# Performance work log

Hardware: AMD Instinct MI355X
Metric: run time of the kernel (lower is better)

The kernel has to match this reference:

```python
import jax, jax.numpy as jnp
import numpy as np

N_NODES = 50000
N_EDGES = 600000
HEADS = 4
DH = 64
NUM_GRAPHS = 8
NEG_SLOPE = 0.2


def setup_inputs() -> dict:
    key = jax.random.key(0)
    ks = jax.random.split(key, 10)
    feat = jax.random.normal(ks[0], (N_NODES, 128), jnp.float32)
    W0 = jax.random.normal(ks[1], (128, HEADS * DH), jnp.float32) * 0.05
    W1 = jax.random.normal(ks[2], (HEADS * DH, HEADS * DH), jnp.float32) * 0.05
    W2 = jax.random.normal(ks[3], (HEADS * DH, HEADS * DH), jnp.float32) * 0.05
    a0 = jax.random.normal(ks[4], (HEADS, DH), jnp.float32) * 0.05
    a1 = jax.random.normal(ks[5], (HEADS, DH), jnp.float32) * 0.05
    a2 = jax.random.normal(ks[6], (HEADS, DH), jnp.float32) * 0.05
    src = jax.random.randint(ks[7], (N_EDGES,), 0, N_NODES, jnp.int32)
    dst = jax.random.randint(ks[8], (N_EDGES,), 0, N_NODES, jnp.int32)
    graph_ids = jnp.sort(jax.random.randint(ks[9], (N_NODES,), 0, NUM_GRAPHS, jnp.int32))
    return {"feat": feat, "W0": W0, "W1": W1, "W2": W2,
            "a0": a0, "a1": a1, "a2": a2,
            "src": src, "dst": dst, "graph_ids": graph_ids}


def _gatv2_layer(h, W, a, src, dst, residual):
    # DGL GATv2Conv with share_weights=True, bias=False, activation=elu.
    n = h.shape[0]
    feat = (h @ W).reshape(n, HEADS, DH)               # (N,H,D)
    # GATv2 attention: score_ij = a . leaky_relu(W h_i + W h_j)
    e = jax.nn.leaky_relu(feat[src] + feat[dst], NEG_SLOPE)  # (E,H,D)
    scores = jnp.einsum('ehd,hd->eh', e, a)            # (E,H)
    # edge softmax over incoming edges of each dst node
    m = jnp.full((n, HEADS), -jnp.inf, scores.dtype).at[dst].max(scores)
    ex = jnp.exp(scores - m[dst])
    denom = jnp.zeros((n, HEADS), scores.dtype).at[dst].add(ex)
    alpha = ex / denom[dst]                            # (E,H)
    out = jnp.zeros((n, HEADS, DH), h.dtype).at[dst].add(alpha[..., None] * feat[src])
    if residual:
        out = out + h.reshape(n, HEADS, DH)            # identity residual (in == H*D)
    return jax.nn.elu(out).reshape(n, HEADS * DH)      # flatten(1)


def reference(feat, W0, W1, W2, a0, a1, a2, src, dst, graph_ids):
    h = _gatv2_layer(feat, W0, a0, src, dst, residual=False)
    h = _gatv2_layer(h, W1, a1, src, dst, residual=True)
    h = _gatv2_layer(h, W2, a2, src, dst, residual=True)
    # dgl.mean_nodes: per-graph mean over nodes
    sums = jax.ops.segment_sum(h, graph_ids, num_segments=NUM_GRAPHS)
    counts = jax.ops.segment_sum(jnp.ones((h.shape[0],), h.dtype), graph_ids,
                                 num_segments=NUM_GRAPHS)
    return sums / jnp.maximum(counts, 1.0)[:, None]    # (NUM_GRAPHS, H*D)
```

## Files before the change

### kernel.cpp

```cpp
#include <hip/hip_runtime.h>
#include <math.h>

#define N_NODES 50000
#define N_EDGES 600000
#define HD 256
#define NUM_GRAPHS 8
#define POOL_CHUNK 128
#define L2E 1.4426950408889634f

static inline size_t align256(size_t x) { return (x + 255) & ~(size_t)255; }

typedef __attribute__((ext_vector_type(8))) short short8;
typedef __attribute__((ext_vector_type(8))) unsigned short u16x8;
typedef __attribute__((ext_vector_type(4))) float f32x4;

__device__ inline float b2f(unsigned short u) {
    union { unsigned int i; float f; } v; v.i = ((unsigned)u) << 16; return v.f;
}
__device__ inline unsigned short f2b(float f) {
    unsigned int u = __float_as_uint(f);
    unsigned int r = (u + 0x7fff + ((u >> 16) & 1)) >> 16;
    return (unsigned short)r;
}

#define CNT_BLOCKS ((N_EDGES + 255) / 256)
__global__ void prep_kernel(const int* __restrict__ dst, int* __restrict__ cnt,
                            const float* __restrict__ W0, const float* __restrict__ W1,
                            const float* __restrict__ W2,
                            unsigned short* __restrict__ Wt0, unsigned short* __restrict__ Wt1,
                            unsigned short* __restrict__ Wt2) {
    __shared__ float t[16][17];
    int b = blockIdx.x;
    if (b < CNT_BLOCKS) {
        int e = b * 256 + threadIdx.x;
        if (e < N_EDGES) atomicAdd(&cnt[dst[e]], 1);
        return;
    }
    b -= CNT_BLOCKS;
    const float* W;
    unsigned short* Wt;
    int K;
    if (b < 128) { W = W0; Wt = Wt0; K = 128; }
    else if (b < 128 + 256) { b -= 128; W = W1; Wt = Wt1; K = 256; }
    else { b -= 384; W = W2; Wt = Wt2; K = 256; }
    const int ktiles = K >> 4;
    const int kt = (b % ktiles) * 16;
    const int nt = (b / ktiles) * 16;
    const int tx = threadIdx.x & 15;
    const int ty = threadIdx.x >> 4;
    t[ty][tx] = W[(size_t)(kt + ty) * HD + nt + tx];
    __syncthreads();
    Wt[(size_t)(nt + ty) * K + kt + tx] = f2b(t[tx][ty]);
}

#define SCAN_BLOCKS ((N_NODES + 256) / 256)
__global__ __launch_bounds__(256) void partial_kernel(const int* __restrict__ cnt,
                                                      int* __restrict__ bsum) {
    __shared__ int ws[4];
    const int lane = threadIdx.x & 63;
    const int wid = threadIdx.x >> 6;
    int i = blockIdx.x * 256 + threadIdx.x;
    int v = (i < N_NODES) ? cnt[i] : 0;
#pragma unroll
    for (int ofs = 32; ofs >= 1; ofs >>= 1) v += __shfl_xor(v, ofs);
    if (lane == 0) ws[wid] = v;
    __syncthreads();
    if (threadIdx.x == 0) bsum[blockIdx.x] = ws[0] + ws[1] + ws[2] + ws[3];
}

__global__ __launch_bounds__(256) void scan2_kernel(const int* __restrict__ cnt,
                                                    const int* __restrict__ bsum,
                                                    int* __restrict__ row_ptr,
                                                    int* __restrict__ cursor) {
    __shared__ int wsum[4];
    __shared__ int s_off;
    const int t = threadIdx.x;
    const int lane = t & 63;
    const int wid = t >> 6;
    const int b = blockIdx.x;
    if (wid == 0) {
        int acc = 0;
        for (int j = lane; j < b; j += 64) acc += bsum[j];
#pragma unroll
        for (int ofs = 32; ofs >= 1; ofs >>= 1) acc += __shfl_xor(acc, ofs);
        if (lane == 0) s_off = acc;
    }
    int i = b * 256 + t;
    int v = (i < N_NODES) ? cnt[i] : 0;
    int x = v;
#pragma unroll
    for (int ofs = 1; ofs < 64; ofs <<= 1) {
        int u = __shfl_up(x, ofs);
        if (lane >= ofs) x += u;
    }
    if (lane == 63) wsum[wid] = x;
    __syncthreads();
    int woff = 0;
#pragma unroll
    for (int j = 0; j < 4; ++j) if (j < wid) woff += wsum[j];
    int excl = s_off + woff + x - v;
    if (i <= N_NODES) { row_ptr[i] = excl; cursor[i] = excl; }
}

__global__ void fill_kernel(const int* __restrict__ src, const int* __restrict__ dst,
                            int* __restrict__ cursor, int* __restrict__ col_src) {
    int e = blockIdx.x * blockDim.x + threadIdx.x;
    if (e < N_EDGES) {
        int d = dst[e];
        int slot = atomicAdd(&cursor[d], 1);
        col_src[slot] = src[e];
    }
}

template<int K, bool AF32>
__global__ __launch_bounds__(256) void mfma_gemm(const void* __restrict__ Ap,
                                                 const unsigned short* __restrict__ Wt,
                                                 unsigned short* __restrict__ C) {
    const int tid = threadIdx.x;
    const int lane = tid & 63;
    const int wave = tid >> 6;
    const int lm = lane & 15;
    const int lk = lane >> 4;
    const int row0 = blockIdx.x * 64;
    const int col0 = wave * 64;

    f32x4 acc[4][4];
#pragma unroll
    for (int rt = 0; rt < 4; ++rt)
#pragma unroll
        for (int ct = 0; ct < 4; ++ct) acc[rt][ct] = (f32x4)(0.f);

    int arow[4];
#pragma unroll
    for (int rt = 0; rt < 4; ++rt) {
        int r = row0 + rt * 16 + lm;
        arow[rt] = r < N_NODES ? r : N_NODES - 1;
    }

    const unsigned short* Ab = (const unsigned short*)Ap;
    const float* Af = (const float*)Ap;

#pragma unroll 2
    for (int k0 = 0; k0 < K; k0 += 32) {
        short8 af[4], bfr[4];
#pragma unroll
        for (int rt = 0; rt < 4; ++rt) {
            if constexpr (AF32) {
                const float* p = &Af[(size_t)arow[rt] * K + k0 + lk * 8];
                float4 v0 = *reinterpret_cast<const float4*>(p);
                float4 v1 = *reinterpret_cast<const float4*>(p + 4);
                short8 a;
                a[0] = (short)f2b(v0.x); a[1] = (short)f2b(v0.y);
                a[2] = (short)f2b(v0.z); a[3] = (short)f2b(v0.w);
                a[4] = (short)f2b(v1.x); a[5] = (short)f2b(v1.y);
                a[6] = (short)f2b(v1.z); a[7] = (short)f2b(v1.w);
                af[rt] = a;
            } else {
                af[rt] = *reinterpret_cast<const short8*>(&Ab[(size_t)arow[rt] * K + k0 + lk * 8]);
            }
        }
#pragma unroll
        for (int ct = 0; ct < 4; ++ct)
            bfr[ct] = *reinterpret_cast<const short8*>(
                &Wt[(size_t)(col0 + ct * 16 + lm) * K + k0 + lk * 8]);
#pragma unroll
        for (int ct = 0; ct < 4; ++ct)
#pragma unroll
            for (int rt = 0; rt < 4; ++rt)
                acc[rt][ct] = __builtin_amdgcn_mfma_f32_16x16x32_bf16(af[rt], bfr[ct], acc[rt][ct], 0, 0, 0);
    }

#pragma unroll
    for (int rt = 0; rt < 4; ++rt)
#pragma unroll
        for (int i = 0; i < 4; ++i) {
            int row = row0 + rt * 16 + lk * 4 + i;
            if (row < N_NODES) {
#pragma unroll
                for (int ct = 0; ct < 4; ++ct)
                    C[(size_t)row * HD + col0 + ct * 16 + lm] = f2b(acc[rt][ct][i]);
            }
        }
}

__global__ __launch_bounds__(256) void aggregate_kernel(
        const unsigned short* __restrict__ feat,
        const float* __restrict__ avec,
        const int* __restrict__ row_ptr,
        const int* __restrict__ col_src,
        unsigned short* __restrict__ hb,
        int residual) {
    const int lane = threadIdx.x & 63;
    const int wave = threadIdx.x >> 6;
    const int half = lane >> 5;
    const int sl = lane & 31;
    const int c0 = sl * 8;
    int n0 = blockIdx.x * 4 + wave;
    if (n0 >= N_NODES) return;
    const int n = __builtin_amdgcn_readfirstlane(n0);

    float av6[8], av4[8];
    {
        float4 v0 = *reinterpret_cast<const float4*>(&avec[c0]);
        float4 v1 = *reinterpret_cast<const float4*>(&avec[c0 + 4]);
        float a[8] = {v0.x, v0.y, v0.z, v0.w, v1.x, v1.y, v1.z, v1.w};
#pragma unroll
        for (int k = 0; k < 8; ++k) {
            av6[k] = a[k] * (0.6f * L2E);
            av4[k] = a[k] * (0.4f * L2E);
        }
    }

    float fd[8];
    {
        u16x8 g = *reinterpret_cast<const u16x8*>(&feat[(size_t)n * HD + c0]);
#pragma unroll
        for (int k = 0; k < 8; ++k) fd[k] = b2f(g[k]);
    }

    const int beg = row_ptr[n];
    const int end = row_ptr[n + 1];

    float denom = 0.f;
    float acc[8];
#pragma unroll
    for (int k = 0; k < 8; ++k) acc[k] = 0.f;

    for (int s = beg; s < end; s += 4) {
        int e0 = col_src[s];
        int e1 = col_src[s + 1];
        int e2 = col_src[s + 2];
        int e3 = col_src[s + 3];
        int eP = half ? e1 : e0;
        int eQ = half ? e3 : e2;
        u16x8 g0 = *reinterpret_cast<const u16x8*>(&feat[(size_t)eP * HD + c0]);
        u16x8 g1 = *reinterpret_cast<const u16x8*>(&feat[(size_t)eQ * HD + c0]);

        float sv0[8], sv1[8];
        float pp0 = 0.f, pp1 = 0.f;
#pragma unroll
        for (int k = 0; k < 8; ++k) {
            sv0[k] = b2f(g0[k]);
            float t = sv0[k] + fd[k];
            pp0 = fmaf(av6[k], t, fmaf(av4[k], fabsf(t), pp0));
        }
#pragma unroll
        for (int k = 0; k < 8; ++k) {
            sv1[k] = b2f(g1[k]);
            float t = sv1[k] + fd[k];
            pp1 = fmaf(av6[k], t, fmaf(av4[k], fabsf(t), pp1));
        }
        pp0 += __shfl_xor(pp0, 1); pp1 += __shfl_xor(pp1, 1);
        pp0 += __shfl_xor(pp0, 2); pp1 += __shfl_xor(pp1, 2);
        pp0 += __shfl_xor(pp0, 4); pp1 += __shfl_xor(pp1, 4);

        float w0 = (s + half < end) ? exp2f(pp0) : 0.f;
        float w1 = (s + 2 + half < end) ? exp2f(pp1) : 0.f;
        denom += w0 + w1;
#pragma unroll
        for (int k = 0; k < 8; ++k)
            acc[k] = fmaf(w0, sv0[k], fmaf(w1, sv1[k], acc[k]));
    }

    denom += __shfl_xor(denom, 32);
#pragma unroll
    for (int k = 0; k < 8; ++k) acc[k] += __shfl_xor(acc[k], 32);

    if (half == 0) {
        const float inv = denom > 0.f ? 1.f / denom : 0.f;
        float o[8];
#pragma unroll
        for (int k = 0; k < 8; ++k) o[k] = acc[k] * inv;
        if (residual) {
            u16x8 hr = *reinterpret_cast<const u16x8*>(&hb[(size_t)n * HD + c0]);
#pragma unroll
            for (int k = 0; k < 8; ++k) o[k] += b2f(hr[k]);
        }
        u16x8 ob;
#pragma unroll
        for (int k = 0; k < 8; ++k) {
            float e = o[k] > 0.f ? o[k] : exp2f(o[k] * L2E) - 1.f;
            ob[k] = f2b(e);
        }
        *reinterpret_cast<u16x8*>(&hb[(size_t)n * HD + c0]) = ob;
    }
}

__global__ __launch_bounds__(256) void pool_kernel(const unsigned short* __restrict__ h,
                                                   const int* __restrict__ gid,
                                                   float* __restrict__ gsums,
                                                   int* __restrict__ gcnt) {
    const int t = threadIdx.x;
    int n0 = blockIdx.x * POOL_CHUNK;
    if (n0 >= N_NODES) return;
    int n1 = n0 + POOL_CHUNK; if (n1 > N_NODES) n1 = N_NODES;
    int curg = gid[n0];
    float sum = 0.f;
    int cnt = 0;
    for (int n = n0; n < n1; ++n) {
        int g = gid[n];
        if (g != curg) {
            atomicAdd(&gsums[(size_t)curg * HD + t], sum);
            if (t == 0) atomicAdd(&gcnt[curg], cnt);
            sum = 0.f; cnt = 0; curg = g;
        }
        sum += b2f(h[(size_t)n * HD + t]);
        ++cnt;
    }
    atomicAdd(&gsums[(size_t)curg * HD + t], sum);
    if (t == 0) atomicAdd(&gcnt[curg], cnt);
}

__global__ void finalize_kernel(const float* __restrict__ gsums,
                                const int* __restrict__ gcnt,
                                float* __restrict__ out) {
    int i = blockIdx.x * blockDim.x + threadIdx.x;
    if (i < NUM_GRAPHS * HD) {
        float c = (float)gcnt[i / HD];
        out[i] = gsums[i] / fmaxf(c, 1.f);
    }
}

extern "C" void kernel_launch(void* const* d_in, const int* in_sizes, int n_in,
                              void* d_out, int out_size, void* d_ws, size_t ws_size,
                              hipStream_t stream) {
    (void)in_sizes; (void)n_in;
    const float* feat = (const float*)d_in[0];
    const float* W0 = (const float*)d_in[1];
    const float* W1 = (const float*)d_in[2];
    const float* W2 = (const float*)d_in[3];
    const float* a0 = (const float*)d_in[4];
    const float* a1 = (const float*)d_in[5];
    const float* a2 = (const float*)d_in[6];
    const int* src = (const int*)d_in[7];
    const int* dst = (const int*)d_in[8];
    const int* gid = (const int*)d_in[9];
    float* out = (float*)d_out;

    char* ws = (char*)d_ws;
    size_t off = 0;
    unsigned short* hb = (unsigned short*)(ws + off);  off = align256(off + (size_t)N_NODES * HD * 2);
    unsigned short* Bh = (unsigned short*)(ws + off);  off = align256(off + (size_t)N_NODES * HD * 2);
    unsigned short* Wt0 = (unsigned short*)(ws + off); off = align256(off + (size_t)HD * 128 * 2);
    unsigned short* Wt1 = (unsigned short*)(ws + off); off = align256(off + (size_t)HD * HD * 2);
    unsigned short* Wt2 = (unsigned short*)(ws + off); off = align256(off + (size_t)HD * HD * 2);
    int* row_ptr = (int*)(ws + off);                   off = align256(off + (size_t)(N_NODES + 1) * 4);
    int* cursor = (int*)(ws + off);                    off = align256(off + (size_t)(N_NODES + 1) * 4);
    int* bsum = (int*)(ws + off);                      off = align256(off + (size_t)SCAN_BLOCKS * 4);
    int* col_src = (int*)(ws + off);                   off = off + (size_t)N_EDGES * 4;
    size_t zstart = off;
    off = align256(off + 16 * 4);
    int* cnt = (int*)(ws + off);                       off = align256(off + (size_t)(N_NODES + 1) * 4);
    float* gsums = (float*)(ws + off);                 off = align256(off + (size_t)NUM_GRAPHS * HD * 4);
    int* gcnt = (int*)(ws + off);                      off = align256(off + (size_t)NUM_GRAPHS * 4);
    size_t zend = off;

    if (ws_size < off) {
        hipMemsetAsync(d_out, 0, (size_t)out_size * 4, stream);
        return;
    }

    hipMemsetAsync(ws + zstart, 0, zend - zstart, stream);

    prep_kernel<<<CNT_BLOCKS + 128 + 256 + 256, 256, 0, stream>>>(
        dst, cnt, W0, W1, W2, Wt0, Wt1, Wt2);
    partial_kernel<<<SCAN_BLOCKS, 256, 0, stream>>>(cnt, bsum);
    scan2_kernel<<<SCAN_BLOCKS, 256, 0, stream>>>(cnt, bsum, row_ptr, cursor);
    fill_kernel<<<(N_EDGES + 255) / 256, 256, 0, stream>>>(src, dst, cursor, col_src);

    const int gemm_blocks = (N_NODES + 63) / 64;
    const int agg_blocks = (N_NODES + 3) / 4;

    mfma_gemm<128, true><<<gemm_blocks, 256, 0, stream>>>(feat, Wt0, Bh);
    aggregate_kernel<<<agg_blocks, 256, 0, stream>>>(Bh, a0, row_ptr, col_src, hb, 0);
    mfma_gemm<256, false><<<gemm_blocks, 256, 0, stream>>>(hb, Wt1, Bh);
    aggregate_kernel<<<agg_blocks, 256, 0, stream>>>(Bh, a1, row_ptr, col_src, hb, 1);
    mfma_gemm<256, false><<<gemm_blocks, 256, 0, stream>>>(hb, Wt2, Bh);
    aggregate_kernel<<<agg_blocks, 256, 0, stream>>>(Bh, a2, row_ptr, col_src, hb, 1);

    pool_kernel<<<(N_NODES + POOL_CHUNK - 1) / POOL_CHUNK, 256, 0, stream>>>(hb, gid, gsums, gcnt);
    finalize_kernel<<<(NUM_GRAPHS * HD + 255) / 256, 256, 0, stream>>>(gsums, gcnt, out);
}
```

Before: 365.0 us.

## Split aggregation into three node-range launches, shrink pool chunk, split score FMAs

Each aggregation layer now runs as three launches over node ranges (0..T1, T1..T2, T2..N) instead of one. The likely aim is to keep each launch's destination working set and row pointer accesses more cache-local. The gathered source features stay random, so the benefit is uncertain, and the split adds launch overhead and a tail at the end of each launch. The score dot product now uses two independent accumulators to shorten the FMA dependency chain, and the pooling chunk shrinks from 128 to 32 nodes to launch more blocks.

```diff
diff --git a/kernel.cpp b/kernel.cpp
--- a/kernel.cpp
+++ b/kernel.cpp
@@ -5,7 +5,7 @@
 #define N_EDGES 600000
 #define HD 256
 #define NUM_GRAPHS 8
-#define POOL_CHUNK 128
+#define POOL_CHUNK 32
 #define L2E 1.4426950408889634f
 
 static inline size_t align256(size_t x) { return (x + 255) & ~(size_t)255; }
@@ -189,14 +189,14 @@
         const int* __restrict__ row_ptr,
         const int* __restrict__ col_src,
         unsigned short* __restrict__ hb,
-        int residual) {
+        int residual, int nbase, int nlim) {
     const int lane = threadIdx.x & 63;
     const int wave = threadIdx.x >> 6;
     const int half = lane >> 5;
     const int sl = lane & 31;
     const int c0 = sl * 8;
-    int n0 = blockIdx.x * 4 + wave;
-    if (n0 >= N_NODES) return;
+    int n0 = nbase + blockIdx.x * 4 + wave;
+    if (n0 >= nlim) return;
     const int n = __builtin_amdgcn_readfirstlane(n0);
 
     float av6[8], av4[8];
@@ -237,19 +237,23 @@
         u16x8 g1 = *reinterpret_cast<const u16x8*>(&feat[(size_t)eQ * HD + c0]);
 
         float sv0[8], sv1[8];
-        float pp0 = 0.f, pp1 = 0.f;
+        float pa0 = 0.f, pb0 = 0.f, pa1 = 0.f, pb1 = 0.f;
 #pragma unroll
         for (int k = 0; k < 8; ++k) {
             sv0[k] = b2f(g0[k]);
             float t = sv0[k] + fd[k];
-            pp0 = fmaf(av6[k], t, fmaf(av4[k], fabsf(t), pp0));
+            pa0 = fmaf(av6[k], t, pa0);
+            pb0 = fmaf(av4[k], fabsf(t), pb0);
         }
 #pragma unroll
         for (int k = 0; k < 8; ++k) {
             sv1[k] = b2f(g1[k]);
             float t = sv1[k] + fd[k];
-            pp1 = fmaf(av6[k], t, fmaf(av4[k], fabsf(t), pp1));
-        }
+            pa1 = fmaf(av6[k], t, pa1);
+            pb1 = fmaf(av4[k], fabsf(t), pb1);
+        }
+        float pp0 = pa0 + pb0;
+        float pp1 = pa1 + pb1;
         pp0 += __shfl_xor(pp0, 1); pp1 += __shfl_xor(pp1, 1);
         pp0 += __shfl_xor(pp0, 2); pp1 += __shfl_xor(pp1, 2);
         pp0 += __shfl_xor(pp0, 4); pp1 += __shfl_xor(pp1, 4);
@@ -369,14 +373,24 @@
     fill_kernel<<<(N_EDGES + 255) / 256, 256, 0, stream>>>(src, dst, cursor, col_src);
 
     const int gemm_blocks = (N_NODES + 63) / 64;
-    const int agg_blocks = (N_NODES + 3) / 4;
+    const int T1 = 16668, T2 = 33336;
+    const int agg_blocks = (T1 + 3) / 4;
+
+#define AGG_LAYER(FEAT, AV, RES)                                                        \
+    aggregate_kernel<<<agg_blocks, 256, 0, stream>>>(FEAT, AV, row_ptr, col_src, hb,    \
+                                                     RES, 0, T1);                       \
+    aggregate_kernel<<<agg_blocks, 256, 0, stream>>>(FEAT, AV, row_ptr, col_src, hb,    \
+                                                     RES, T1, T2);                      \
+    aggregate_kernel<<<agg_blocks, 256, 0, stream>>>(FEAT, AV, row_ptr, col_src, hb,    \
+                                                     RES, T2, N_NODES);
 
     mfma_gemm<128, true><<<gemm_blocks, 256, 0, stream>>>(feat, Wt0, Bh);
-    aggregate_kernel<<<agg_blocks, 256, 0, stream>>>(Bh, a0, row_ptr, col_src, hb, 0);
+    AGG_LAYER(Bh, a0, 0)
     mfma_gemm<256, false><<<gemm_blocks, 256, 0, stream>>>(hb, Wt1, Bh);
-    aggregate_kernel<<<agg_blocks, 256, 0, stream>>>(Bh, a1, row_ptr, col_src, hb, 1);
+    AGG_LAYER(Bh, a1, 1)
     mfma_gemm<256, false><<<gemm_blocks, 256, 0, stream>>>(hb, Wt2, Bh);
-    aggregate_kernel<<<agg_blocks, 256, 0, stream>>>(Bh, a2, row_ptr, col_src, hb, 1);
+    AGG_LAYER(Bh, a2, 1)
+#undef AGG_LAYER
 
     pool_kernel<<<(N_NODES + POOL_CHUNK - 1) / POOL_CHUNK, 256, 0, stream>>>(hb, gid, gsums, gcnt);
     finalize_kernel<<<(NUM_GRAPHS * HD + 255) / 256, 256, 0, stream>>>(gsums, gcnt, out);
```

Result: slower. 399.1 us (+9.4%).

## Fuse edge aggregation with the next layer's GEMM in one kernel

Applied to the files above, without the earlier changes.

Adds agg_gemm_kernel, where 16 waves each aggregate one node, write the ELU output to hb and to an LDS tile, then run a 16x256 MFMA against the next layer's weights. This removes two standalone GEMM launches and the HBM round-trip that re-read hb, and ping-pongs between two feature buffers so a kernel never reads what it writes. In exchange, the fused GEMM runs small 16-row tiles that reload the whole weight matrix from global for every block, and the 1024-thread blocks with a barrier may reduce occupancy.

```diff
diff --git a/kernel.cpp b/kernel.cpp
--- a/kernel.cpp
+++ b/kernel.cpp
@@ -183,6 +183,127 @@
         }
 }
 
+__global__ __launch_bounds__(1024) void agg_gemm_kernel(
+        const unsigned short* __restrict__ feat,
+        const float* __restrict__ avec,
+        const int* __restrict__ row_ptr,
+        const int* __restrict__ col_src,
+        unsigned short* __restrict__ hb,
+        const unsigned short* __restrict__ Wt,
+        unsigned short* __restrict__ feat_out,
+        int residual) {
+    __shared__ unsigned short hrow[16][264];
+    const int tid = threadIdx.x;
+    const int wave = tid >> 6;
+    const int lane = tid & 63;
+    const int half = lane >> 5;
+    const int sl = lane & 31;
+    const int c0 = sl * 8;
+    const int n = __builtin_amdgcn_readfirstlane(blockIdx.x * 16 + wave);
+
+    float av6[8], av4[8];
+    {
+        float4 v0 = *reinterpret_cast<const float4*>(&avec[c0]);
+        float4 v1 = *reinterpret_cast<const float4*>(&avec[c0 + 4]);
+        float a[8] = {v0.x, v0.y, v0.z, v0.w, v1.x, v1.y, v1.z, v1.w};
+#pragma unroll
+        for (int k = 0; k < 8; ++k) {
+            av6[k] = a[k] * (0.6f * L2E);
+            av4[k] = a[k] * (0.4f * L2E);
+        }
+    }
+    float fd[8];
+    {
+        u16x8 g = *reinterpret_cast<const u16x8*>(&feat[(size_t)n * HD + c0]);
+#pragma unroll
+        for (int k = 0; k < 8; ++k) fd[k] = b2f(g[k]);
+    }
+    const int beg = row_ptr[n];
+    const int end = row_ptr[n + 1];
+
+    float denom = 0.f;
+    float acc[8];
+#pragma unroll
+    for (int k = 0; k < 8; ++k) acc[k] = 0.f;
+
+    for (int s = beg; s < end; s += 4) {
+        int e0 = col_src[s];
+        int e1 = col_src[s + 1];
+        int e2 = col_src[s + 2];
+        int e3 = col_src[s + 3];
+        int eP = half ? e1 : e0;
+        int eQ = half ? e3 : e2;
+        u16x8 g0 = *reinterpret_cast<const u16x8*>(&feat[(size_t)eP * HD + c0]);
+        u16x8 g1 = *reinterpret_cast<const u16x8*>(&feat[(size_t)eQ * HD + c0]);
+
+        float sv0[8], sv1[8];
+        float pp0 = 0.f, pp1 = 0.f;
+#pragma unroll
+        for (int k = 0; k < 8; ++k) {
+            sv0[k] = b2f(g0[k]);
+            float t = sv0[k] + fd[k];
+            pp0 = fmaf(av6[k], t, fmaf(av4[k], fabsf(t), pp0));
+        }
+#pragma unroll
+        for (int k = 0; k < 8; ++k) {
+            sv1[k] = b2f(g1[k]);
+            float t = sv1[k] + fd[k];
+            pp1 = fmaf(av6[k], t, fmaf(av4[k], fabsf(t), pp1));
+        }
+        pp0 += __shfl_xor(pp0, 1); pp1 += __shfl_xor(pp1, 1);
+        pp0 += __shfl_xor(pp0, 2); pp1 += __shfl_xor(pp1, 2);
+        pp0 += __shfl_xor(pp0, 4); pp1 += __shfl_xor(pp1, 4);
+
+        float w0 = (s + half < end) ? exp2f(pp0) : 0.f;
+        float w1 = (s + 2 + half < end) ? exp2f(pp1) : 0.f;
+        denom += w0 + w1;
+#pragma unroll
+        for (int k = 0; k < 8; ++k)
+            acc[k] = fmaf(w0, sv0[k], fmaf(w1, sv1[k], acc[k]));
+    }
+
+    denom += __shfl_xor(denom, 32);
+#pragma unroll
+    for (int k = 0; k < 8; ++k) acc[k] += __shfl_xor(acc[k], 32);
+
+    if (half == 0) {
+        const float inv = denom > 0.f ? 1.f / denom : 0.f;
+        float o[8];
+#pragma unroll
+        for (int k = 0; k < 8; ++k) o[k] = acc[k] * inv;
+        if (residual) {
+            u16x8 hr = *reinterpret_cast<const u16x8*>(&hb[(size_t)n * HD + c0]);
+#pragma unroll
+            for (int k = 0; k < 8; ++k) o[k] += b2f(hr[k]);
+        }
+        u16x8 ob;
+#pragma unroll
+        for (int k = 0; k < 8; ++k) {
+            float e = o[k] > 0.f ? o[k] : exp2f(o[k] * L2E) - 1.f;
+            ob[k] = f2b(e);
+        }
+        *reinterpret_cast<u16x8*>(&hb[(size_t)n * HD + c0]) = ob;
+        *reinterpret_cast<u16x8*>(&hrow[wave][c0]) = ob;
+    }
+    __syncthreads();
+
+    const int lm = lane & 15;
+    const int lk = lane >> 4;
+    const int col0 = wave * 16;
+    f32x4 gacc = (f32x4)(0.f);
+#pragma unroll
+    for (int kk = 0; kk < 8; ++kk) {
+        short8 afr = *reinterpret_cast<const short8*>(&hrow[lm][kk * 32 + lk * 8]);
+        short8 bfr = *reinterpret_cast<const short8*>(
+            &Wt[(size_t)(col0 + lm) * 256 + kk * 32 + lk * 8]);
+        gacc = __builtin_amdgcn_mfma_f32_16x16x32_bf16(afr, bfr, gacc, 0, 0, 0);
+    }
+    const int rowb = blockIdx.x * 16 + lk * 4;
+#pragma unroll
+    for (int i = 0; i < 4; ++i)
+        feat_out[(size_t)(rowb + i) * HD + col0 + lm] = f2b(gacc[i]);
+}
+
 __global__ __launch_bounds__(256) void aggregate_kernel(
         const unsigned short* __restrict__ feat,
         const float* __restrict__ avec,
@@ -210,14 +331,12 @@
             av4[k] = a[k] * (0.4f * L2E);
         }
     }
-
     float fd[8];
     {
         u16x8 g = *reinterpret_cast<const u16x8*>(&feat[(size_t)n * HD + c0]);
 #pragma unroll
         for (int k = 0; k < 8; ++k) fd[k] = b2f(g[k]);
     }
-
     const int beg = row_ptr[n];
     const int end = row_ptr[n + 1];
 
@@ -339,20 +458,21 @@
 
     char* ws = (char*)d_ws;
     size_t off = 0;
-    unsigned short* hb = (unsigned short*)(ws + off);  off = align256(off + (size_t)N_NODES * HD * 2);
-    unsigned short* Bh = (unsigned short*)(ws + off);  off = align256(off + (size_t)N_NODES * HD * 2);
-    unsigned short* Wt0 = (unsigned short*)(ws + off); off = align256(off + (size_t)HD * 128 * 2);
-    unsigned short* Wt1 = (unsigned short*)(ws + off); off = align256(off + (size_t)HD * HD * 2);
-    unsigned short* Wt2 = (unsigned short*)(ws + off); off = align256(off + (size_t)HD * HD * 2);
-    int* row_ptr = (int*)(ws + off);                   off = align256(off + (size_t)(N_NODES + 1) * 4);
-    int* cursor = (int*)(ws + off);                    off = align256(off + (size_t)(N_NODES + 1) * 4);
-    int* bsum = (int*)(ws + off);                      off = align256(off + (size_t)SCAN_BLOCKS * 4);
-    int* col_src = (int*)(ws + off);                   off = off + (size_t)N_EDGES * 4;
+    unsigned short* hb = (unsigned short*)(ws + off);   off = align256(off + (size_t)N_NODES * HD * 2);
+    unsigned short* BhA = (unsigned short*)(ws + off);  off = align256(off + (size_t)N_NODES * HD * 2);
+    unsigned short* BhB = (unsigned short*)(ws + off);  off = align256(off + (size_t)N_NODES * HD * 2);
+    unsigned short* Wt0 = (unsigned short*)(ws + off);  off = align256(off + (size_t)HD * 128 * 2);
+    unsigned short* Wt1 = (unsigned short*)(ws + off);  off = align256(off + (size_t)HD * HD * 2);
+    unsigned short* Wt2 = (unsigned short*)(ws + off);  off = align256(off + (size_t)HD * HD * 2);
+    int* row_ptr = (int*)(ws + off);                    off = align256(off + (size_t)(N_NODES + 1) * 4);
+    int* cursor = (int*)(ws + off);                     off = align256(off + (size_t)(N_NODES + 1) * 4);
+    int* bsum = (int*)(ws + off);                       off = align256(off + (size_t)SCAN_BLOCKS * 4);
+    int* col_src = (int*)(ws + off);                    off = off + (size_t)N_EDGES * 4;
     size_t zstart = off;
     off = align256(off + 16 * 4);
-    int* cnt = (int*)(ws + off);                       off = align256(off + (size_t)(N_NODES + 1) * 4);
-    float* gsums = (float*)(ws + off);                 off = align256(off + (size_t)NUM_GRAPHS * HD * 4);
-    int* gcnt = (int*)(ws + off);                      off = align256(off + (size_t)NUM_GRAPHS * 4);
+    int* cnt = (int*)(ws + off);                        off = align256(off + (size_t)(N_NODES + 1) * 4);
+    float* gsums = (float*)(ws + off);                  off = align256(off + (size_t)NUM_GRAPHS * HD * 4);
+    int* gcnt = (int*)(ws + off);                       off = align256(off + (size_t)NUM_GRAPHS * 4);
     size_t zend = off;
 
     if (ws_size < off) {
@@ -369,14 +489,13 @@
     fill_kernel<<<(N_EDGES + 255) / 256, 256, 0, stream>>>(src, dst, cursor, col_src);
 
     const int gemm_blocks = (N_NODES + 63) / 64;
+    const int aggg_blocks = N_NODES / 16;
     const int agg_blocks = (N_NODES + 3) / 4;
 
-    mfma_gemm<128, true><<<gemm_blocks, 256, 0, stream>>>(feat, Wt0, Bh);
-    aggregate_kernel<<<agg_blocks, 256, 0, stream>>>(Bh, a0, row_ptr, col_src, hb, 0);
-    mfma_gemm<256, false><<<gemm_blocks, 256, 0, stream>>>(hb, Wt1, Bh);
-    aggregate_kernel<<<agg_blocks, 256, 0, stream>>>(Bh, a1, row_ptr, col_src, hb, 1);
-    mfma_gemm<256, false><<<gemm_blocks, 256, 0, stream>>>(hb, Wt2, Bh);
-    aggregate_kernel<<<agg_blocks, 256, 0, stream>>>(Bh, a2, row_ptr, col_src, hb, 1);
+    mfma_gemm<128, true><<<gemm_blocks, 256, 0, stream>>>(feat, Wt0, BhA);
+    agg_gemm_kernel<<<aggg_blocks, 1024, 0, stream>>>(BhA, a0, row_ptr, col_src, hb, Wt1, BhB, 0);
+    agg_gemm_kernel<<<aggg_blocks, 1024, 0, stream>>>(BhB, a1, row_ptr, col_src, hb, Wt2, BhA, 1);
+    aggregate_kernel<<<agg_blocks, 256, 0, stream>>>(BhA, a2, row_ptr, col_src, hb, 1);
 
     pool_kernel<<<(N_NODES + POOL_CHUNK - 1) / POOL_CHUNK, 256, 0, stream>>>(hb, gid, gsums, gcnt);
     finalize_kernel<<<(NUM_GRAPHS * HD + 255) / 256, 256, 0, stream>>>(gsums, gcnt, out);
```

New measurement: 419.6 us. 1.15x slower.
